# Kernel tuning notes

Hardware: AMD Instinct MI355X
Metric: run time of the kernel (lower is better)

## Reference

```python
import jax, jax.numpy as jnp
import numpy as np

B, N, C, H, EMB = 4, 2048, 1024, 16, 1024
D = C // H            # head dim = 64
MLP = 4 * C           # 4096
INNER = int(np.floor(C * 4.0 * (2.0 / 3.0)))  # SwiGLU parity inner = 2730
EPS = 1e-5

def layer_norm(x, w, b):
    mu = jnp.mean(x, axis=-1, keepdims=True)
    var = jnp.mean((x - mu) ** 2, axis=-1, keepdims=True)
    return (x - mu) * jax.lax.rsqrt(var + EPS) * w + b

def setup_inputs() -> dict:
    key = jax.random.key(0)
    ks = jax.random.split(key, 16)
    def p(i, shape, scale=0.02):
        return jax.random.normal(ks[i], shape, jnp.float32) * scale
    return dict(
        x=p(0, (B, N, C), 1.0),
        emb=p(1, (B, N, EMB), 1.0),
        W_emb=p(2, (EMB, 2 * C)), b_emb=jnp.zeros((2 * C,), jnp.float32),
        ln_w=jnp.ones((C,), jnp.float32), ln_b=jnp.zeros((C,), jnp.float32),
        W_f=p(3, (C, 3 * C + MLP)), b_f=p(4, (3 * C + MLP,)),
        qn_w=jnp.ones((D,), jnp.float32), qn_b=jnp.zeros((D,), jnp.float32),
        kn_w=jnp.ones((D,), jnp.float32), kn_b=jnp.zeros((D,), jnp.float32),
        W_ao=p(5, (C, C)), b_ao=p(6, (C,)),
        W_mo=p(7, (MLP, C)), b_mo=p(8, (C,)),
        Wm_in=p(9, (C, 2 * INNER)), bm_in=p(10, (2 * INNER,)),
        Wm_out=p(11, (INNER, C)), bm_out=p(12, (C,)),
        W_g=p(13, (C, H)), b_g=p(14, (H,)),
    )

def reference(x, emb, W_emb, b_emb, ln_w, ln_b, W_f, b_f, qn_w, qn_b,
              kn_w, kn_b, W_ao, b_ao, W_mo, b_mo, Wm_in, bm_in,
              Wm_out, bm_out, W_g, b_g):
    Bn, Nn, Cn = x.shape
    _x = x
    # FiLM conditioning: LN(x) * (1+scale) + shift
    se = emb @ W_emb + b_emb
    scale, shift = se[..., :Cn], se[..., Cn:]
    xn = layer_norm(x, ln_w, ln_b) * (1.0 + scale) + shift
    # fused qkv + mlp projection
    fused = xn @ W_f + b_f
    qkv = fused[..., :3 * Cn]
    mlp_h = fused[..., 3 * Cn:]
    qkv = qkv.reshape(Bn, Nn, 3, H, D).transpose(2, 0, 3, 1, 4)  # (3,b,h,n,d)
    q, k, v = qkv[0], qkv[1], qkv[2]
    q = layer_norm(q, qn_w, qn_b)
    k = layer_norm(k, kn_w, kn_b)
    q_prior = q  # rope is None
    # scaled dot product attention (no mask)
    logits = jnp.einsum('bhnd,bhmd->bhnm', q, k) / jnp.sqrt(jnp.float32(D))
    attn = jax.nn.softmax(logits, axis=-1)
    o = jnp.einsum('bhnm,bhmd->bhnd', attn, v)
    # KV-memory branch: SwiGLU(q_prior), detached, rms-normalized per (b,h), gated
    qp = q_prior.transpose(0, 2, 1, 3).reshape(Bn, Nn, Cn)  # b n (h d)
    vg = qp @ Wm_in + bm_in
    vv, g = vg[..., :INNER], vg[..., INNER:]
    f = (jax.nn.silu(g) * vv) @ Wm_out + bm_out
    f = jax.lax.stop_gradient(f)
    f = f.reshape(Bn, Nn, H, D).transpose(0, 2, 1, 3)  # b h n d
    rms = jnp.maximum(jnp.sqrt(jnp.mean(f ** 2, axis=(-1, -2), keepdims=True)), 1e-6)
    f = f / rms
    gate = jnp.tanh(_x @ W_g + b_g)            # (b, n, h)
    gate = gate.transpose(0, 2, 1)[..., None]  # (b, h, n, 1)
    o = o + gate * f
    o = o.transpose(0, 2, 1, 3).reshape(Bn, Nn, Cn)  # b n (h d)
    x2 = _x + (o @ W_ao + b_ao)
    out = x2 + (jax.nn.silu(mlp_h) @ W_mo + b_mo)
    return out
```

## Files before the change

### kernel.cpp

```cpp
#include <hip/hip_runtime.h>
#include <hip/hip_bf16.h>
#include <cstdint>
#include <cstddef>

#define B_    4
#define N_    2048
#define C_    1024
#define H_    16
#define D_    64
#define TOK   (B_ * N_)
#define MLP_  4096
#define INNER_   2730
#define INNER_P  2752
#define NG_      5460
#define NG_P     5504

typedef unsigned short u16;
typedef __attribute__((ext_vector_type(4))) float f32x4;
typedef __attribute__((ext_vector_type(8))) short bf16x8;

#define MFMA_BF16(a, b, c) __builtin_amdgcn_mfma_f32_16x16x32_bf16((a), (b), (c), 0, 0, 0)

__device__ __forceinline__ u16 f2bf(float f) {
    union { float f; unsigned u; } v; v.f = f;
    unsigned r = v.u + 0x7FFFu + ((v.u >> 16) & 1u);
    return (u16)(r >> 16);
}
__device__ __forceinline__ float bf2f(u16 u) {
    union { float f; unsigned u; } v; v.u = ((unsigned)u) << 16; return v.f;
}
__device__ __forceinline__ ushort4 bf4(float a, float b, float c, float d) {
    ushort4 o; o.x = f2bf(a); o.y = f2bf(b); o.z = f2bf(c); o.w = f2bf(d); return o;
}

__global__ __launch_bounds__(256)
void tb_transpose_bf16(const float* __restrict__ W, u16* __restrict__ Wt,
                       int K, int N, int Kp, int Np) {
    __shared__ float tile[32][33];
    const int k0 = blockIdx.x * 32, n0 = blockIdx.y * 32;
    const int t = threadIdx.x;
    const int r = t >> 3, c0 = (t & 7) * 4;
#pragma unroll
    for (int i = 0; i < 4; i++) {
        int k = k0 + r, n = n0 + c0 + i;
        tile[r][c0 + i] = (k < K && n < N) ? W[(size_t)k * N + n] : 0.f;
    }
    __syncthreads();
#pragma unroll
    for (int i = 0; i < 4; i++) {
        Wt[(size_t)(n0 + r) * Kp + k0 + c0 + i] = f2bf(tile[c0 + i][r]);
    }
}

__global__ __launch_bounds__(256)
void tb_transpose_glu(const float* __restrict__ W, u16* __restrict__ Wt) {
    __shared__ float tv[32][17], tg[32][17];
    const int k0 = blockIdx.x * 32, r0 = blockIdx.y * 32;
    const int s0 = r0 >> 1;
    const int t = threadIdx.x;
    const int kk = t >> 3, j0 = (t & 7) * 2;
#pragma unroll
    for (int i = 0; i < 2; i++) {
        int j = j0 + i, k = k0 + kk;
        int cV = s0 + j, cG = INNER_ + s0 + j;
        tv[kk][j] = (cV < INNER_) ? W[(size_t)k * NG_ + cV] : 0.f;
        tg[kk][j] = (cG < NG_)    ? W[(size_t)k * NG_ + cG] : 0.f;
    }
    __syncthreads();
    const int r = t >> 3, c0 = (t & 7) * 4;
#pragma unroll
    for (int i = 0; i < 4; i++) {
        int k = c0 + i;
        float v = (r & 1) ? tg[k][r >> 1] : tv[k][r >> 1];
        Wt[(size_t)(r0 + r) * 1024 + k0 + k] = f2bf(v);
    }
}

__global__ __launch_bounds__(256)
void tb_conv_bf16(const float* __restrict__ in, u16* __restrict__ out, int n4) {
    int i = blockIdx.x * 256 + threadIdx.x;
    const int stride = gridDim.x * 256;
    for (; i < n4; i += stride) {
        f32x4 v = ((const f32x4*)in)[i];
        ((ushort4*)out)[i] = bf4(v.x, v.y, v.z, v.w);
    }
}

__global__ __launch_bounds__(256)
void tb_bias_glu(const float* __restrict__ b, float* __restrict__ bp) {
    int r = blockIdx.x * 256 + threadIdx.x;
    if (r < NG_P) {
        int i = r >> 1;
        float v = 0.f;
        if (i < INNER_) v = (r & 1) ? b[INNER_ + i] : b[i];
        bp[r] = v;
    }
}

template <int EPI>
__global__ __launch_bounds__(256)
void tb_gemm(const u16* __restrict__ A, const u16* __restrict__ Bt,
             const float* __restrict__ bias, const float* add,
             float* outf, u16* outb,
             int M, int N, int K, int lda, int ldb, int ldc) {
    __shared__ u16 As[128 * 32];
    __shared__ u16 Bs[128 * 32];
    const int tid = threadIdx.x;
    const int l = tid & 63, w = tid >> 6;
    const int wr = w >> 1, wc = w & 1;
    const int fr = l & 15, fq = l >> 4;
    const int ntn = N >> 7;
    const int bm0 = (blockIdx.x / ntn) << 7;
    const int bn0 = (blockIdx.x % ntn) << 7;

    const int c0 = tid, c1 = tid + 256;
    const int ar0 = c0 >> 2, ak0 = (c0 & 3) * 8;
    const int ar1 = c1 >> 2, ak1 = (c1 & 3) * 8;

    const u16* Ab = A + (size_t)bm0 * lda;
    const u16* Bb = Bt + (size_t)bn0 * ldb;

    f32x4 acc[4][4] = {};

    bf16x8 ra0 = *(const bf16x8*)(Ab + (size_t)ar0 * lda + ak0);
    bf16x8 ra1 = *(const bf16x8*)(Ab + (size_t)ar1 * lda + ak1);
    bf16x8 rb0 = *(const bf16x8*)(Bb + (size_t)ar0 * ldb + ak0);
    bf16x8 rb1 = *(const bf16x8*)(Bb + (size_t)ar1 * ldb + ak1);

    const int nk = K >> 5;
    for (int kt = 0; kt < nk; kt++) {
        __syncthreads();
        ((bf16x8*)As)[c0] = ra0; ((bf16x8*)As)[c1] = ra1;
        ((bf16x8*)Bs)[c0] = rb0; ((bf16x8*)Bs)[c1] = rb1;
        __syncthreads();
        if (kt + 1 < nk) {
            const int k0 = (kt + 1) << 5;
            ra0 = *(const bf16x8*)(Ab + (size_t)ar0 * lda + k0 + ak0);
            ra1 = *(const bf16x8*)(Ab + (size_t)ar1 * lda + k0 + ak1);
            rb0 = *(const bf16x8*)(Bb + (size_t)ar0 * ldb + k0 + ak0);
            rb1 = *(const bf16x8*)(Bb + (size_t)ar1 * ldb + k0 + ak1);
        }
        bf16x8 af[4], bfr[4];
#pragma unroll
        for (int mi = 0; mi < 4; mi++)
            af[mi] = ((const bf16x8*)As)[(wr * 64 + mi * 16 + fr) * 4 + fq];
#pragma unroll
        for (int ni = 0; ni < 4; ni++)
            bfr[ni] = ((const bf16x8*)Bs)[(wc * 64 + ni * 16 + fr) * 4 + fq];
#pragma unroll
        for (int mi = 0; mi < 4; mi++)
#pragma unroll
            for (int ni = 0; ni < 4; ni++)
                acc[mi][ni] = MFMA_BF16(af[mi], bfr[ni], acc[mi][ni]);
    }

#pragma unroll
    for (int mi = 0; mi < 4; mi++) {
#pragma unroll
        for (int ni = 0; ni < 4; ni++) {
            const int row0 = bm0 + wr * 64 + mi * 16 + fq * 4;
            const int col  = bn0 + wc * 64 + ni * 16 + fr;
            const float bc = bias[col];
#pragma unroll
            for (int j = 0; j < 4; j++) {
                float v = acc[mi][ni][j] + bc;
                if constexpr (EPI == 1) {
                    size_t oi = (size_t)(row0 + j) * ldc + col;
                    outf[oi] = v + add[oi];
                } else if constexpr (EPI == 3) {
                    outb[(size_t)(row0 + j) * ldc + col] = f2bf(v);
                } else if constexpr (EPI == 5) {
                    float s = v * (1.f / (1.f + __expf(-v)));
                    outb[(size_t)(row0 + j) * ldc + col] = f2bf(s);
                } else {
                    float partner = __shfl_xor(v, 1, 64);
                    if ((fr & 1) == 0) {
                        float g = partner;
                        float a = g * (1.f / (1.f + __expf(-g))) * v;
                        outb[(size_t)(row0 + j) * ldc + (col >> 1)] = f2bf(a);
                    }
                }
            }
        }
    }
}

__global__ __launch_bounds__(256)
void tb_ln_mod(const float* __restrict__ x, const u16* __restrict__ se,
               const float* __restrict__ lw, const float* __restrict__ lb,
               u16* __restrict__ xn) {
    const int tok = blockIdx.x;
    const int t = threadIdx.x;
    f32x4 v = ((const f32x4*)(x + (size_t)tok * 1024))[t];
    float s = v.x + v.y + v.z + v.w;
    float ss = v.x * v.x + v.y * v.y + v.z * v.z + v.w * v.w;
#pragma unroll
    for (int m = 1; m < 64; m <<= 1) {
        s += __shfl_xor(s, m, 64);
        ss += __shfl_xor(ss, m, 64);
    }
    __shared__ float sb[4], ssb[4];
    if ((t & 63) == 0) { sb[t >> 6] = s; ssb[t >> 6] = ss; }
    __syncthreads();
    s = sb[0] + sb[1] + sb[2] + sb[3];
    ss = ssb[0] + ssb[1] + ssb[2] + ssb[3];
    const float mu = s * (1.f / 1024.f);
    const float var = ss * (1.f / 1024.f) - mu * mu;
    const float rs = rsqrtf(var + 1e-5f);
    f32x4 w4 = ((const f32x4*)lw)[t];
    f32x4 b4 = ((const f32x4*)lb)[t];
    const u16* ser = se + (size_t)tok * 2048;
    ushort4 scu = ((const ushort4*)ser)[t];
    ushort4 shu = ((const ushort4*)(ser + 1024))[t];
    float y0 = ((v.x - mu) * rs * w4.x + b4.x) * (1.f + bf2f(scu.x)) + bf2f(shu.x);
    float y1 = ((v.y - mu) * rs * w4.y + b4.y) * (1.f + bf2f(scu.y)) + bf2f(shu.y);
    float y2 = ((v.z - mu) * rs * w4.z + b4.z) * (1.f + bf2f(scu.z)) + bf2f(shu.z);
    float y3 = ((v.w - mu) * rs * w4.w + b4.w) * (1.f + bf2f(scu.w)) + bf2f(shu.w);
    ((ushort4*)xn)[(size_t)tok * 256 + t] = bf4(y0, y1, y2, y3);
}

__global__ __launch_bounds__(256)
void tb_qkv_ln(const u16* __restrict__ qkv,
               const float* __restrict__ qw, const float* __restrict__ qb,
               const float* __restrict__ kw, const float* __restrict__ kb,
               u16* __restrict__ qo, u16* __restrict__ ko, u16* __restrict__ vo) {
    const int tok = blockIdx.x;
    const int t = threadIdx.x;
    const int h = t >> 4, ln16 = t & 15;
    const u16* base = qkv + (size_t)tok * 3072 + h * 64 + ln16 * 4;
    ushort4 qu = *(const ushort4*)(base);
    ushort4 ku = *(const ushort4*)(base + 1024);
    ushort4 vu = *(const ushort4*)(base + 2048);
    float q0 = bf2f(qu.x), q1 = bf2f(qu.y), q2 = bf2f(qu.z), q3 = bf2f(qu.w);
    float k0 = bf2f(ku.x), k1 = bf2f(ku.y), k2 = bf2f(ku.z), k3 = bf2f(ku.w);
    float qs = q0 + q1 + q2 + q3, qss = q0 * q0 + q1 * q1 + q2 * q2 + q3 * q3;
    float ks = k0 + k1 + k2 + k3, kss = k0 * k0 + k1 * k1 + k2 * k2 + k3 * k3;
#pragma unroll
    for (int m = 1; m < 16; m <<= 1) {
        qs += __shfl_xor(qs, m, 64); qss += __shfl_xor(qss, m, 64);
        ks += __shfl_xor(ks, m, 64); kss += __shfl_xor(kss, m, 64);
    }
    const float qmu = qs * (1.f / 64.f), kmu = ks * (1.f / 64.f);
    const float qrs = rsqrtf(qss * (1.f / 64.f) - qmu * qmu + 1e-5f);
    const float krs = rsqrtf(kss * (1.f / 64.f) - kmu * kmu + 1e-5f);
    f32x4 qw4 = ((const f32x4*)qw)[ln16], qb4 = ((const f32x4*)qb)[ln16];
    f32x4 kw4 = ((const f32x4*)kw)[ln16], kb4 = ((const f32x4*)kb)[ln16];
    const size_t oidx = (((size_t)tok * 16 + h) * 64 + ln16 * 4) >> 2;
    ((ushort4*)qo)[oidx] = bf4((q0 - qmu) * qrs * qw4.x + qb4.x, (q1 - qmu) * qrs * qw4.y + qb4.y,
                               (q2 - qmu) * qrs * qw4.z + qb4.z, (q3 - qmu) * qrs * qw4.w + qb4.w);
    ((ushort4*)ko)[oidx] = bf4((k0 - kmu) * krs * kw4.x + kb4.x, (k1 - kmu) * krs * kw4.y + kb4.y,
                               (k2 - kmu) * krs * kw4.z + kb4.z, (k3 - kmu) * krs * kw4.w + kb4.w);
    ((ushort4*)vo)[oidx] = vu;
}

__global__ __launch_bounds__(256)
void tb_attn(const u16* __restrict__ q, const u16* __restrict__ k,
             const u16* __restrict__ v, u16* __restrict__ o) {
    const int qb = blockIdx.x, bh = blockIdx.y;
    const int b = bh >> 4, h = bh & 15;
    const int t = threadIdx.x, l = t & 63, w = t >> 6;
    const int fr = l & 15, fq = l >> 4;
    __shared__ u16 VT[64 * 72];
    __shared__ u16 P[4][16 * 72];

    const int q0 = qb * 64 + w * 16;
    const u16* qp = q + (size_t)b * N_ * 1024 + h * 64;
    const u16* kp = k + (size_t)b * N_ * 1024 + h * 64;
    const u16* vp = v + (size_t)b * N_ * 1024 + h * 64;

    bf16x8 aq[2];
    aq[0] = *(const bf16x8*)(qp + (size_t)(q0 + fr) * 1024 + fq * 8);
    aq[1] = *(const bf16x8*)(qp + (size_t)(q0 + fr) * 1024 + 32 + fq * 8);

    float m_r[4], l_r[4];
    f32x4 oa[4];
#pragma unroll
    for (int r = 0; r < 4; r++) { m_r[r] = -1e30f; l_r[r] = 0.f; }
#pragma unroll
    for (int c = 0; c < 4; c++) oa[c] = f32x4{0.f, 0.f, 0.f, 0.f};

    for (int kt = 0; kt < N_ / 64; kt++) {
        const int kv0 = kt * 64;
#pragma unroll
        for (int i = 0; i < 16; i++) {
            int lin = i * 256 + t;
            int kvr = lin >> 6, d = lin & 63;
            VT[d * 72 + kvr] = vp[(size_t)(kv0 + kvr) * 1024 + d];
        }
        __syncthreads();
        f32x4 sfr[4];
#pragma unroll
        for (int c = 0; c < 4; c++) {
            bf16x8 bk0 = *(const bf16x8*)(kp + (size_t)(kv0 + c * 16 + fr) * 1024 + fq * 8);
            bf16x8 bk1 = *(const bf16x8*)(kp + (size_t)(kv0 + c * 16 + fr) * 1024 + 32 + fq * 8);
            f32x4 sa = {};
            sa = MFMA_BF16(aq[0], bk0, sa);
            sa = MFMA_BF16(aq[1], bk1, sa);
            sfr[c] = sa * 0.125f;
        }
        float alpha[4];
#pragma unroll
        for (int r = 0; r < 4; r++) {
            float mx = fmaxf(fmaxf(sfr[0][r], sfr[1][r]), fmaxf(sfr[2][r], sfr[3][r]));
#pragma unroll
            for (int mm = 1; mm < 16; mm <<= 1) mx = fmaxf(mx, __shfl_xor(mx, mm, 64));
            float nm = fmaxf(m_r[r], mx);
            alpha[r] = __expf(m_r[r] - nm);
            m_r[r] = nm;
        }
        float rs[4] = {0.f, 0.f, 0.f, 0.f};
#pragma unroll
        for (int c = 0; c < 4; c++) {
#pragma unroll
            for (int r = 0; r < 4; r++) {
                float p = __expf(sfr[c][r] - m_r[r]);
                rs[r] += p;
                P[w][(fq * 4 + r) * 72 + c * 16 + fr] = f2bf(p);
            }
        }
#pragma unroll
        for (int r = 0; r < 4; r++) {
#pragma unroll
            for (int mm = 1; mm < 16; mm <<= 1) rs[r] += __shfl_xor(rs[r], mm, 64);
            l_r[r] = l_r[r] * alpha[r] + rs[r];
        }
#pragma unroll
        for (int c2 = 0; c2 < 4; c2++) {
            oa[c2][0] *= alpha[0]; oa[c2][1] *= alpha[1];
            oa[c2][2] *= alpha[2]; oa[c2][3] *= alpha[3];
        }
#pragma unroll
        for (int kk = 0; kk < 2; kk++) {
            bf16x8 pa = *(const bf16x8*)&P[w][fr * 72 + kk * 32 + fq * 8];
#pragma unroll
            for (int c2 = 0; c2 < 4; c2++) {
                bf16x8 vbb = *(const bf16x8*)&VT[(c2 * 16 + fr) * 72 + kk * 32 + fq * 8];
                oa[c2] = MFMA_BF16(pa, vbb, oa[c2]);
            }
        }
        __syncthreads();
    }
    u16* op = o + (size_t)b * N_ * 1024 + h * 64;
#pragma unroll
    for (int c2 = 0; c2 < 4; c2++)
#pragma unroll
        for (int r = 0; r < 4; r++)
            op[(size_t)(q0 + fq * 4 + r) * 1024 + c2 * 16 + fr] = f2bf(oa[c2][r] / l_r[r]);
}

__global__ __launch_bounds__(256)
void tb_rms_reduce(const u16* __restrict__ f, float* __restrict__ rbuf) {
    const int bid = blockIdx.x;
    const int bh = bid >> 4, part = bid & 15;
    const int b = bh >> 4, h = bh & 15;
    const int t = threadIdx.x;
    const int d = t & 63, nn = t >> 6;
    const u16* fp = f + (size_t)b * N_ * 1024 + h * 64 + d;
    float s = 0.f;
#pragma unroll 4
    for (int i = 0; i < 32; i++) {
        int n = part * 128 + nn + i * 4;
        float v = bf2f(fp[(size_t)n * 1024]);
        s += v * v;
    }
#pragma unroll
    for (int m = 1; m < 64; m <<= 1) s += __shfl_xor(s, m, 64);
    __shared__ float sb[4];
    if ((t & 63) == 0) sb[t >> 6] = s;
    __syncthreads();
    if (t == 0) atomicAdd(&rbuf[bh], sb[0] + sb[1] + sb[2] + sb[3]);
}

__global__ __launch_bounds__(256)
void tb_gate(const float* __restrict__ x, const float* __restrict__ Wg,
             const float* __restrict__ bg, float* __restrict__ gate) {
    const int tok = blockIdx.x;
    const int t = threadIdx.x;
    const int h = t & 15, part = t >> 4;
    const float* xr = x + (size_t)tok * 1024 + part * 64;
    float s = 0.f;
#pragma unroll 8
    for (int c = 0; c < 64; c++) s += xr[c] * Wg[(size_t)(part * 64 + c) * 16 + h];
    s += __shfl_xor(s, 16, 64);
    s += __shfl_xor(s, 32, 64);
    __shared__ float gb[4][16];
    if ((t & 63) < 16) gb[t >> 6][t & 15] = s;
    __syncthreads();
    if (t < 16) gate[(size_t)tok * 16 + t] = tanhf(gb[0][t] + gb[1][t] + gb[2][t] + gb[3][t] + bg[t]);
}

__global__ __launch_bounds__(256)
void tb_combine(const u16* __restrict__ o, const u16* __restrict__ f,
                const float* __restrict__ gate, const float* __restrict__ rbuf,
                u16* __restrict__ ob) {
    const int i = blockIdx.x * 256 + threadIdx.x;
    const int idx4 = i * 4;
    const int h = (idx4 >> 6) & 15;
    const int tok = idx4 >> 10;
    const int b = idx4 >> 21;
    const float g = gate[(size_t)tok * 16 + h];
    float r = rbuf[(b << 4) + h];
    r = fmaxf(sqrtf(r * (1.f / 131072.f)), 1e-6f);
    const float inv = g / r;
    ushort4 ou = ((const ushort4*)o)[i];
    ushort4 fu = ((const ushort4*)f)[i];
    float r0 = bf2f(ou.x) + bf2f(fu.x) * inv;
    float r1 = bf2f(ou.y) + bf2f(fu.y) * inv;
    float r2 = bf2f(ou.z) + bf2f(fu.z) * inv;
    float r3 = bf2f(ou.w) + bf2f(fu.w) * inv;
    ((ushort4*)ob)[i] = bf4(r0, r1, r2, r3);
}

extern "C" void kernel_launch(void* const* d_in, const int* in_sizes, int n_in,
                              void* d_out, int out_size, void* d_ws, size_t ws_size,
                              hipStream_t stream) {
    const float* x      = (const float*)d_in[0];
    const float* emb    = (const float*)d_in[1];
    const float* W_emb  = (const float*)d_in[2];
    const float* b_emb  = (const float*)d_in[3];
    const float* ln_w   = (const float*)d_in[4];
    const float* ln_b   = (const float*)d_in[5];
    const float* W_f    = (const float*)d_in[6];
    const float* b_f    = (const float*)d_in[7];
    const float* qn_w   = (const float*)d_in[8];
    const float* qn_b   = (const float*)d_in[9];
    const float* kn_w   = (const float*)d_in[10];
    const float* kn_b   = (const float*)d_in[11];
    const float* W_ao   = (const float*)d_in[12];
    const float* b_ao   = (const float*)d_in[13];
    const float* W_mo   = (const float*)d_in[14];
    const float* b_mo   = (const float*)d_in[15];
    const float* Wm_in  = (const float*)d_in[16];
    const float* bm_in  = (const float*)d_in[17];
    const float* Wm_out = (const float*)d_in[18];
    const float* bm_out = (const float*)d_in[19];
    const float* W_g    = (const float*)d_in[20];
    const float* b_g    = (const float*)d_in[21];
    float* out = (float*)d_out;
    char* ws = (char*)d_ws;
    (void)ws_size; (void)n_in; (void)in_sizes; (void)out_size;

    size_t off = 0;
    auto alloc = [&](size_t bytes) { size_t o = off; off += (bytes + 255) & ~(size_t)255; return o; };
    const size_t oWfT    = alloc((size_t)7168 * 1024 * 2);
    const size_t oWminT  = alloc((size_t)NG_P * 1024 * 2);
    const size_t oWmoutT = alloc((size_t)1024 * INNER_P * 2);
    const size_t oWaoT   = alloc((size_t)1024 * 1024 * 2);
    const size_t oWmoT   = alloc((size_t)1024 * 4096 * 2);
    const size_t oWembT  = alloc((size_t)2048 * 1024 * 2);
    const size_t oEmbB   = alloc((size_t)TOK * 1024 * 2);
    const size_t oY      = alloc((size_t)TOK * 3072 * 2);
    const size_t oZql    = alloc((size_t)TOK * 1024 * 2);
    const size_t oZkl    = alloc((size_t)TOK * 1024 * 2);
    const size_t oZvb    = alloc((size_t)TOK * 1024 * 2);
    const size_t oXN     = alloc((size_t)TOK * 1024 * 2);
    const size_t oBias   = alloc((size_t)NG_P * 4);
    const size_t oGate   = alloc((size_t)TOK * 16 * 4);
    const size_t oRms    = alloc((size_t)64 * 4);

    u16* WfT    = (u16*)(ws + oWfT);
    u16* WminT  = (u16*)(ws + oWminT);
    u16* WmoutT = (u16*)(ws + oWmoutT);
    u16* WaoT   = (u16*)(ws + oWaoT);
    u16* WmoT   = (u16*)(ws + oWmoT);
    u16* WembT  = (u16*)(ws + oWembT);
    u16* embB   = (u16*)(ws + oEmbB);
    u16* se     = (u16*)(ws + oY);
    u16* qkv    = (u16*)(ws + oY);
    u16* act    = (u16*)(ws + oY);
    u16* sm     = (u16*)(ws + oY);
    u16* ql     = (u16*)(ws + oZql);
    u16* kl     = (u16*)(ws + oZkl);
    u16* fbuf   = (u16*)(ws + oZkl);
    u16* vb     = (u16*)(ws + oZvb);
    u16* ob     = (u16*)(ws + oZvb);
    u16* obuf   = (u16*)(ws + oWembT);
    u16* xn     = (u16*)(ws + oXN);
    float* biasP = (float*)(ws + oBias);
    float* gate = (float*)(ws + oGate);
    float* rms  = (float*)(ws + oRms);

    hipLaunchKernelGGL(tb_transpose_bf16, dim3(32, 64),  dim3(256), 0, stream, W_emb,  WembT,  1024, 2048, 1024, 2048);
    hipLaunchKernelGGL(tb_transpose_bf16, dim3(32, 224), dim3(256), 0, stream, W_f,    WfT,    1024, 7168, 1024, 7168);
    hipLaunchKernelGGL(tb_transpose_glu,  dim3(32, 172), dim3(256), 0, stream, Wm_in,  WminT);
    hipLaunchKernelGGL(tb_transpose_bf16, dim3(86, 32),  dim3(256), 0, stream, Wm_out, WmoutT, INNER_, 1024, INNER_P, 1024);
    hipLaunchKernelGGL(tb_transpose_bf16, dim3(32, 32),  dim3(256), 0, stream, W_ao,   WaoT,   1024, 1024, 1024, 1024);
    hipLaunchKernelGGL(tb_transpose_bf16, dim3(128, 32), dim3(256), 0, stream, W_mo,   WmoT,   4096, 1024, 4096, 1024);
    hipLaunchKernelGGL(tb_conv_bf16, dim3(4096), dim3(256), 0, stream, emb, embB, TOK * 1024 / 4);
    hipLaunchKernelGGL(tb_bias_glu, dim3((NG_P + 255) / 256), dim3(256), 0, stream, bm_in, biasP);
    hipMemsetAsync(rms, 0, 64 * sizeof(float), stream);

    hipLaunchKernelGGL((tb_gemm<3>), dim3(64 * 16), dim3(256), 0, stream,
                       embB, WembT, b_emb, nullptr, nullptr, se, TOK, 2048, 1024, 1024, 1024, 2048);
    hipLaunchKernelGGL(tb_ln_mod, dim3(TOK), dim3(256), 0, stream, x, se, ln_w, ln_b, xn);
    hipLaunchKernelGGL((tb_gemm<3>), dim3(64 * 24), dim3(256), 0, stream,
                       xn, WfT, b_f, nullptr, nullptr, qkv, TOK, 3072, 1024, 1024, 1024, 3072);
    hipLaunchKernelGGL(tb_qkv_ln, dim3(TOK), dim3(256), 0, stream, qkv, qn_w, qn_b, kn_w, kn_b, ql, kl, vb);
    hipLaunchKernelGGL(tb_attn, dim3(N_ / 64, B_ * H_), dim3(256), 0, stream, ql, kl, vb, obuf);
    hipLaunchKernelGGL((tb_gemm<4>), dim3(64 * 43), dim3(256), 0, stream,
                       ql, WminT, biasP, nullptr, nullptr, act, TOK, NG_P, 1024, 1024, 1024, INNER_P);
    hipLaunchKernelGGL((tb_gemm<3>), dim3(64 * 8), dim3(256), 0, stream,
                       act, WmoutT, bm_out, nullptr, nullptr, fbuf, TOK, 1024, INNER_P, INNER_P, INNER_P, 1024);
    hipLaunchKernelGGL(tb_rms_reduce, dim3(1024), dim3(256), 0, stream, fbuf, rms);
    hipLaunchKernelGGL(tb_gate, dim3(TOK), dim3(256), 0, stream, x, W_g, b_g, gate);
    hipLaunchKernelGGL(tb_combine, dim3(TOK * 1024 / 4 / 256), dim3(256), 0, stream, obuf, fbuf, gate, rms, ob);
    hipLaunchKernelGGL((tb_gemm<1>), dim3(64 * 8), dim3(256), 0, stream,
                       ob, WaoT, b_ao, x, out, nullptr, TOK, 1024, 1024, 1024, 1024, 1024);
    hipLaunchKernelGGL((tb_gemm<5>), dim3(64 * 32), dim3(256), 0, stream,
                       xn, WfT + (size_t)3072 * 1024, b_f + 3072, nullptr, nullptr, sm,
                       TOK, 4096, 1024, 1024, 1024, 4096);
    hipLaunchKernelGGL((tb_gemm<1>), dim3(64 * 8), dim3(256), 0, stream,
                       sm, WmoT, b_mo, out, out, nullptr, TOK, 1024, 4096, 4096, 4096, 1024);
}
```

Measured before the change: 1.220 ms.

## Use direct global-to-LDS loads in GEMM and restructure attention with pre-transposed V

The GEMM now loads A/B tiles directly into shared memory with global_load_lds instead of staging them through registers, and remaps block IDs across 8 groups, presumably for XCD locality. Attention gets a separate V-transpose kernel, so each block reads V^T from global memory directly instead of doing a scalar LDS transpose with block-wide barriers every tile. It also computes S^T so that softmax reductions need only two shuffles, and remaps blocks for XCD affinity. In exchange the GEMM loses its register prefetch, so load and compute no longer overlap, and attention now reads V from global memory without LDS reuse.

```diff
diff --git a/kernel.cpp b/kernel.cpp
--- a/kernel.cpp
+++ b/kernel.cpp
@@ -32,6 +32,11 @@
 __device__ __forceinline__ ushort4 bf4(float a, float b, float c, float d) {
     ushort4 o; o.x = f2bf(a); o.y = f2bf(b); o.z = f2bf(c); o.w = f2bf(d); return o;
 }
+__device__ __forceinline__ void gld16(const u16* g, u16* l) {
+    __builtin_amdgcn_global_load_lds(
+        (const __attribute__((address_space(1))) void*)(g),
+        (__attribute__((address_space(3))) void*)(l), 16, 0, 0);
+}
 
 __global__ __launch_bounds__(256)
 void tb_transpose_bf16(const float* __restrict__ W, u16* __restrict__ Wt,
@@ -109,37 +114,35 @@
     const int l = tid & 63, w = tid >> 6;
     const int wr = w >> 1, wc = w & 1;
     const int fr = l & 15, fq = l >> 4;
+    int bid = blockIdx.x;
+    const int cpx = gridDim.x >> 3;
+    bid = (bid & 7) * cpx + (bid >> 3);
     const int ntn = N >> 7;
-    const int bm0 = (blockIdx.x / ntn) << 7;
-    const int bn0 = (blockIdx.x % ntn) << 7;
-
-    const int c0 = tid, c1 = tid + 256;
-    const int ar0 = c0 >> 2, ak0 = (c0 & 3) * 8;
-    const int ar1 = c1 >> 2, ak1 = (c1 & 3) * 8;
-
-    const u16* Ab = A + (size_t)bm0 * lda;
-    const u16* Bb = Bt + (size_t)bn0 * ldb;
+    const int bm0 = (bid / ntn) << 7;
+    const int bn0 = (bid % ntn) << 7;
+
+    const int ar0 = tid >> 2, ak0 = (tid & 3) * 8;
+
+    const u16* Ag0 = A + (size_t)(bm0 + ar0) * lda + ak0;
+    const u16* Ag1 = A + (size_t)(bm0 + 64 + ar0) * lda + ak0;
+    const u16* Bg0 = Bt + (size_t)(bn0 + ar0) * ldb + ak0;
+    const u16* Bg1 = Bt + (size_t)(bn0 + 64 + ar0) * ldb + ak0;
+    u16* AsW0 = As + w * 512;
+    u16* AsW1 = As + 2048 + w * 512;
+    u16* BsW0 = Bs + w * 512;
+    u16* BsW1 = Bs + 2048 + w * 512;
 
     f32x4 acc[4][4] = {};
-
-    bf16x8 ra0 = *(const bf16x8*)(Ab + (size_t)ar0 * lda + ak0);
-    bf16x8 ra1 = *(const bf16x8*)(Ab + (size_t)ar1 * lda + ak1);
-    bf16x8 rb0 = *(const bf16x8*)(Bb + (size_t)ar0 * ldb + ak0);
-    bf16x8 rb1 = *(const bf16x8*)(Bb + (size_t)ar1 * ldb + ak1);
 
     const int nk = K >> 5;
     for (int kt = 0; kt < nk; kt++) {
+        const int koff = kt << 5;
         __syncthreads();
-        ((bf16x8*)As)[c0] = ra0; ((bf16x8*)As)[c1] = ra1;
-        ((bf16x8*)Bs)[c0] = rb0; ((bf16x8*)Bs)[c1] = rb1;
+        gld16(Ag0 + koff, AsW0);
+        gld16(Ag1 + koff, AsW1);
+        gld16(Bg0 + koff, BsW0);
+        gld16(Bg1 + koff, BsW1);
         __syncthreads();
-        if (kt + 1 < nk) {
-            const int k0 = (kt + 1) << 5;
-            ra0 = *(const bf16x8*)(Ab + (size_t)ar0 * lda + k0 + ak0);
-            ra1 = *(const bf16x8*)(Ab + (size_t)ar1 * lda + k0 + ak1);
-            rb0 = *(const bf16x8*)(Bb + (size_t)ar0 * ldb + k0 + ak0);
-            rb1 = *(const bf16x8*)(Bb + (size_t)ar1 * ldb + k0 + ak1);
-        }
         bf16x8 af[4], bfr[4];
 #pragma unroll
         for (int mi = 0; mi < 4; mi++)
@@ -254,98 +257,119 @@
 }
 
 __global__ __launch_bounds__(256)
+void tb_vtrans(const u16* __restrict__ v, u16* __restrict__ vt) {
+    __shared__ u16 tile[64][72];
+    const int bh = blockIdx.y, b = bh >> 4, h = bh & 15;
+    const int n0 = blockIdx.x * 64;
+    const int t = threadIdx.x;
+#pragma unroll
+    for (int i = 0; i < 2; i++) {
+        int lin = i * 256 + t;
+        int nl = lin >> 3, d0 = (lin & 7) * 8;
+        bf16x8 val = *(const bf16x8*)(v + (((size_t)b * N_ + n0 + nl) * 16 + h) * 64 + d0);
+        *(bf16x8*)&tile[nl][d0] = val;
+    }
+    __syncthreads();
+#pragma unroll
+    for (int i = 0; i < 2; i++) {
+        int lin = i * 256 + t;
+        int d = lin >> 3, nl0 = (lin & 7) * 8;
+        ushort4 o0, o1;
+        o0.x = tile[nl0 + 0][d]; o0.y = tile[nl0 + 1][d];
+        o0.z = tile[nl0 + 2][d]; o0.w = tile[nl0 + 3][d];
+        o1.x = tile[nl0 + 4][d]; o1.y = tile[nl0 + 5][d];
+        o1.z = tile[nl0 + 6][d]; o1.w = tile[nl0 + 7][d];
+        u16* op = vt + (((size_t)bh * 64) + d) * N_ + n0 + nl0;
+        *(ushort4*)(op) = o0; *(ushort4*)(op + 4) = o1;
+    }
+}
+
+__global__ __launch_bounds__(256)
 void tb_attn(const u16* __restrict__ q, const u16* __restrict__ k,
-             const u16* __restrict__ v, u16* __restrict__ o) {
-    const int qb = blockIdx.x, bh = blockIdx.y;
+             const u16* __restrict__ vt, u16* __restrict__ o) {
+    int lin = blockIdx.y * 32 + blockIdx.x;
+    lin = (lin & 7) * 256 + (lin >> 3);
+    const int bh = lin >> 5, qb = lin & 31;
     const int b = bh >> 4, h = bh & 15;
     const int t = threadIdx.x, l = t & 63, w = t >> 6;
     const int fr = l & 15, fq = l >> 4;
-    __shared__ u16 VT[64 * 72];
     __shared__ u16 P[4][16 * 72];
+    u16* Pw = &P[w][0];
 
     const int q0 = qb * 64 + w * 16;
     const u16* qp = q + (size_t)b * N_ * 1024 + h * 64;
     const u16* kp = k + (size_t)b * N_ * 1024 + h * 64;
-    const u16* vp = v + (size_t)b * N_ * 1024 + h * 64;
-
-    bf16x8 aq[2];
-    aq[0] = *(const bf16x8*)(qp + (size_t)(q0 + fr) * 1024 + fq * 8);
-    aq[1] = *(const bf16x8*)(qp + (size_t)(q0 + fr) * 1024 + 32 + fq * 8);
-
-    float m_r[4], l_r[4];
-    f32x4 oa[4];
-#pragma unroll
-    for (int r = 0; r < 4; r++) { m_r[r] = -1e30f; l_r[r] = 0.f; }
-#pragma unroll
-    for (int c = 0; c < 4; c++) oa[c] = f32x4{0.f, 0.f, 0.f, 0.f};
+    const u16* vp = vt + (size_t)bh * 64 * N_;
+
+    bf16x8 bq[2];
+    bq[0] = *(const bf16x8*)(qp + (size_t)(q0 + fr) * 1024 + fq * 8);
+    bq[1] = *(const bf16x8*)(qp + (size_t)(q0 + fr) * 1024 + 32 + fq * 8);
+
+    float m_s = -1e30f, l_s = 0.f;
+    f32x4 oa[4] = {};
 
     for (int kt = 0; kt < N_ / 64; kt++) {
         const int kv0 = kt * 64;
-#pragma unroll
-        for (int i = 0; i < 16; i++) {
-            int lin = i * 256 + t;
-            int kvr = lin >> 6, d = lin & 63;
-            VT[d * 72 + kvr] = vp[(size_t)(kv0 + kvr) * 1024 + d];
+        f32x4 st[4];
+#pragma unroll
+        for (int c = 0; c < 4; c++) {
+            const u16* krow = kp + (size_t)(kv0 + c * 16 + fr) * 1024;
+            bf16x8 ka0 = *(const bf16x8*)(krow + fq * 8);
+            bf16x8 ka1 = *(const bf16x8*)(krow + 32 + fq * 8);
+            f32x4 sa = {};
+            sa = MFMA_BF16(ka0, bq[0], sa);
+            sa = MFMA_BF16(ka1, bq[1], sa);
+            st[c] = sa * 0.125f;
         }
-        __syncthreads();
-        f32x4 sfr[4];
+        float mx = st[0][0];
+#pragma unroll
+        for (int c = 0; c < 4; c++)
+#pragma unroll
+            for (int r = 0; r < 4; r++) mx = fmaxf(mx, st[c][r]);
+        mx = fmaxf(mx, __shfl_xor(mx, 16, 64));
+        mx = fmaxf(mx, __shfl_xor(mx, 32, 64));
+        const float nm = fmaxf(m_s, mx);
+        const float alpha_q = __expf(m_s - nm);
+        m_s = nm;
+        float lt = 0.f;
 #pragma unroll
         for (int c = 0; c < 4; c++) {
-            bf16x8 bk0 = *(const bf16x8*)(kp + (size_t)(kv0 + c * 16 + fr) * 1024 + fq * 8);
-            bf16x8 bk1 = *(const bf16x8*)(kp + (size_t)(kv0 + c * 16 + fr) * 1024 + 32 + fq * 8);
-            f32x4 sa = {};
-            sa = MFMA_BF16(aq[0], bk0, sa);
-            sa = MFMA_BF16(aq[1], bk1, sa);
-            sfr[c] = sa * 0.125f;
-        }
-        float alpha[4];
-#pragma unroll
-        for (int r = 0; r < 4; r++) {
-            float mx = fmaxf(fmaxf(sfr[0][r], sfr[1][r]), fmaxf(sfr[2][r], sfr[3][r]));
-#pragma unroll
-            for (int mm = 1; mm < 16; mm <<= 1) mx = fmaxf(mx, __shfl_xor(mx, mm, 64));
-            float nm = fmaxf(m_r[r], mx);
-            alpha[r] = __expf(m_r[r] - nm);
-            m_r[r] = nm;
-        }
-        float rs[4] = {0.f, 0.f, 0.f, 0.f};
-#pragma unroll
-        for (int c = 0; c < 4; c++) {
 #pragma unroll
             for (int r = 0; r < 4; r++) {
-                float p = __expf(sfr[c][r] - m_r[r]);
-                rs[r] += p;
-                P[w][(fq * 4 + r) * 72 + c * 16 + fr] = f2bf(p);
+                float p = __expf(st[c][r] - nm);
+                lt += p;
+                Pw[fr * 72 + c * 16 + fq * 4 + r] = f2bf(p);
             }
         }
+        lt += __shfl_xor(lt, 16, 64);
+        lt += __shfl_xor(lt, 32, 64);
+        l_s = l_s * alpha_q + lt;
 #pragma unroll
         for (int r = 0; r < 4; r++) {
-#pragma unroll
-            for (int mm = 1; mm < 16; mm <<= 1) rs[r] += __shfl_xor(rs[r], mm, 64);
-            l_r[r] = l_r[r] * alpha[r] + rs[r];
+            float ao = __shfl(alpha_q, fq * 4 + r, 64);
+#pragma unroll
+            for (int c2 = 0; c2 < 4; c2++) oa[c2][r] *= ao;
         }
-#pragma unroll
-        for (int c2 = 0; c2 < 4; c2++) {
-            oa[c2][0] *= alpha[0]; oa[c2][1] *= alpha[1];
-            oa[c2][2] *= alpha[2]; oa[c2][3] *= alpha[3];
-        }
+        asm volatile("s_waitcnt lgkmcnt(0)" ::: "memory");
 #pragma unroll
         for (int kk = 0; kk < 2; kk++) {
-            bf16x8 pa = *(const bf16x8*)&P[w][fr * 72 + kk * 32 + fq * 8];
+            bf16x8 pa = *(const bf16x8*)&Pw[fr * 72 + kk * 32 + fq * 8];
 #pragma unroll
             for (int c2 = 0; c2 < 4; c2++) {
-                bf16x8 vbb = *(const bf16x8*)&VT[(c2 * 16 + fr) * 72 + kk * 32 + fq * 8];
+                bf16x8 vbb = *(const bf16x8*)(vp + (size_t)(c2 * 16 + fr) * N_ + kv0 + kk * 32 + fq * 8);
                 oa[c2] = MFMA_BF16(pa, vbb, oa[c2]);
             }
         }
-        __syncthreads();
-    }
+    }
+    float lo[4];
+#pragma unroll
+    for (int r = 0; r < 4; r++) lo[r] = __shfl(l_s, fq * 4 + r, 64);
     u16* op = o + (size_t)b * N_ * 1024 + h * 64;
 #pragma unroll
     for (int c2 = 0; c2 < 4; c2++)
 #pragma unroll
         for (int r = 0; r < 4; r++)
-            op[(size_t)(q0 + fq * 4 + r) * 1024 + c2 * 16 + fr] = f2bf(oa[c2][r] / l_r[r]);
+            op[(size_t)(q0 + fq * 4 + r) * 1024 + c2 * 16 + fr] = f2bf(oa[c2][r] / lo[r]);
 }
 
 __global__ __launch_bounds__(256)
@@ -467,6 +491,7 @@
     u16* embB   = (u16*)(ws + oEmbB);
     u16* se     = (u16*)(ws + oY);
     u16* qkv    = (u16*)(ws + oY);
+    u16* vtb    = (u16*)(ws + oY);
     u16* act    = (u16*)(ws + oY);
     u16* sm     = (u16*)(ws + oY);
     u16* ql     = (u16*)(ws + oZql);
@@ -496,7 +521,8 @@
     hipLaunchKernelGGL((tb_gemm<3>), dim3(64 * 24), dim3(256), 0, stream,
                        xn, WfT, b_f, nullptr, nullptr, qkv, TOK, 3072, 1024, 1024, 1024, 3072);
     hipLaunchKernelGGL(tb_qkv_ln, dim3(TOK), dim3(256), 0, stream, qkv, qn_w, qn_b, kn_w, kn_b, ql, kl, vb);
-    hipLaunchKernelGGL(tb_attn, dim3(N_ / 64, B_ * H_), dim3(256), 0, stream, ql, kl, vb, obuf);
+    hipLaunchKernelGGL(tb_vtrans, dim3(32, 64), dim3(256), 0, stream, vb, vtb);
+    hipLaunchKernelGGL(tb_attn, dim3(32, 64), dim3(256), 0, stream, ql, kl, vtb, obuf);
     hipLaunchKernelGGL((tb_gemm<4>), dim3(64 * 43), dim3(256), 0, stream,
                        ql, WminT, biasP, nullptr, nullptr, act, TOK, NG_P, 1024, 1024, 1024, INNER_P);
     hipLaunchKernelGGL((tb_gemm<3>), dim3(64 * 8), dim3(256), 0, stream,
```

Measured after the change: 1.386 ms. +13.6%, slower.
